# Performance work log

Measured on AMD Instinct MI355X. Metric: run time of the kernel, lower is better.

## Reference

```python
import jax, jax.numpy as jnp
import numpy as np

MASK_FILL = -987654321.0


def rotate_every_two(x):
    # pairs (x0, x1) -> (-x1, x0), interleaved back along last dim
    x1 = x[..., 0::2]
    x2 = x[..., 1::2]
    return jnp.stack((-x2, x1), axis=-1).reshape(x.shape)


def setup_inputs() -> dict:
    key = jax.random.key(0)
    ks = jax.random.split(key, 6)
    b, n, dim = 64, 197, 768
    heads, dim_head = 12, 64
    inner = heads * dim_head
    x = jax.random.normal(ks[0], (b, n, dim), dtype=jnp.float32)
    pos_emb = jax.random.normal(ks[1], (1, n, dim_head), dtype=jnp.float32)
    w_qkv = jax.random.normal(ks[2], (dim, 3 * inner), dtype=jnp.float32) * (dim ** -0.5)
    scale = jnp.full((heads,), dim_head ** -0.5, dtype=jnp.float32)
    w_out = jax.random.normal(ks[3], (inner, dim), dtype=jnp.float32) * (inner ** -0.5)
    b_out = jnp.zeros((dim,), dtype=jnp.float32)
    return {"x": x, "pos_emb": pos_emb, "w_qkv": w_qkv, "scale": scale,
            "w_out": w_out, "b_out": b_out}


def reference(x, pos_emb, w_qkv, scale, w_out, b_out):
    b, n, dim = x.shape
    h = scale.shape[0]
    qkv = x @ w_qkv                         # [b, n, 3*inner]
    q, k, v = jnp.split(qkv, 3, axis=-1)
    dh = q.shape[-1] // h
    to_heads = lambda t: t.reshape(b, n, h, dh).transpose(0, 2, 1, 3)  # bhnd
    q, k, v = to_heads(q), to_heads(k), to_heads(v)

    # RoPE: pos_emb [1, n, (2 * dh/2)] -> sin/cos [n, dh/2] -> interleave to [n, dh]
    sc = pos_emb[0].reshape(n, 2, dh // 2)
    sin = jnp.repeat(sc[:, 0], 2, axis=-1)  # [n, dh]
    cos = jnp.repeat(sc[:, 1], 2, axis=-1)
    q = q * cos + rotate_every_two(q) * sin
    k = k * cos + rotate_every_two(k) * sin

    # per-head learnable scale
    dots = jnp.einsum('bhid,bhjd->bhij', q, k) * scale[None, :, None, None]
    # diagonal (LSA) mask
    eye = jnp.eye(n, dtype=bool)
    dots = jnp.where(eye, MASK_FILL, dots)

    attn = jax.nn.softmax(dots, axis=-1)
    out = jnp.einsum('bhij,bhjd->bhid', attn, v)
    out = out.transpose(0, 2, 1, 3).reshape(b, n, h * dh)
    return out @ w_out + b_out
```

## Files before the change

kernel.cpp:

```cpp
#include <hip/hip_runtime.h>
#include <math.h>

#define MASK_FILL_F (-987654321.0f)

typedef unsigned short u16;
typedef unsigned int   u32;

constexpr int Bb   = 64;
constexpr int Ntok = 197;
constexpr int Dim  = 768;
constexpr int Heads= 12;
constexpr int Dh   = 64;
constexpr int Nq3  = 2304;
constexpr int Rows = 12608;
constexpr int Mpad = 12672;

using f32x4  = __attribute__((ext_vector_type(4))) float;
using bf16x8 = __attribute__((ext_vector_type(8))) short;

__device__ __forceinline__ u16 f2bf(float f) {
  u32 u = __float_as_uint(f);
  u = (u + 0x7fffu + ((u >> 16) & 1u)) >> 16;
  return (u16)u;
}

__device__ __forceinline__ void stage16(const void* gp, void* lp) {
  __builtin_amdgcn_global_load_lds(
      (const __attribute__((address_space(1))) u32*)gp,
      (__attribute__((address_space(3))) u32*)lp, 16, 0, 0);
}

__device__ __forceinline__ int sigma6(int M) {
  return (M & 0x23) | (((M >> 3) & 1) << 4) | (((M >> 2) & 1) << 3) |
         (((M >> 4) & 1) << 2);
}

__global__ __launch_bounds__(256) void cvt_bf16(const float* __restrict__ in,
                                                u16* __restrict__ out, int n4) {
  const int i = blockIdx.x * 256 + threadIdx.x;
  if (i < n4) {
    const float4 v = *(const float4*)&in[(size_t)i * 4];
    ushort4 u;
    u.x = f2bf(v.x); u.y = f2bf(v.y); u.z = f2bf(v.z); u.w = f2bf(v.w);
    *(ushort4*)&out[(size_t)i * 4] = u;
  }
}

__global__ __launch_bounds__(256) void transpose_cvt(const float* __restrict__ in,
                                                     u16* __restrict__ out,
                                                     int R, int C) {
  __shared__ float t[32][33];
  const int c0 = blockIdx.x * 32, r0 = blockIdx.y * 32;
  const int tx = threadIdx.x & 31, ty = threadIdx.x >> 5;
#pragma unroll
  for (int rr = ty; rr < 32; rr += 8)
    t[rr][tx] = in[(size_t)(r0 + rr) * C + c0 + tx];
  __syncthreads();
#pragma unroll
  for (int cc = ty; cc < 32; cc += 8)
    out[(size_t)(c0 + cc) * R + r0 + tx] = f2bf(t[tx][cc]);
}

__global__ __launch_bounds__(256) void vtrans(const u16* __restrict__ qkvB,
                                              u16* __restrict__ vT) {
  __shared__ u16 t[64 * 72];
  const int jt = blockIdx.x, bh = blockIdx.y;
  const int b = bh / Heads, h = bh % Heads;
  const int j0 = jt * 64;
  const int tid = threadIdx.x;

  for (int idx = tid; idx < 512; idx += 256) {
    const int jr = idx >> 3, c8 = (idx & 7) * 8;
    const int j = j0 + jr;
    uint4 u = make_uint4(0u, 0u, 0u, 0u);
    if (j < Ntok)
      u = *(const uint4*)(qkvB + (size_t)(b * Ntok + j) * Nq3 + 2 * Dim + h * Dh + c8);
    *(uint4*)&t[jr * 72 + c8] = u;
  }
  __syncthreads();
  for (int idx = tid; idx < 512; idx += 256) {
    const int d = idx >> 3, j8 = (idx & 7) * 8;
    ushort4 lo, hi;
    lo.x = t[(j8 + 0) * 72 + d]; lo.y = t[(j8 + 1) * 72 + d];
    lo.z = t[(j8 + 2) * 72 + d]; lo.w = t[(j8 + 3) * 72 + d];
    hi.x = t[(j8 + 4) * 72 + d]; hi.y = t[(j8 + 5) * 72 + d];
    hi.z = t[(j8 + 6) * 72 + d]; hi.w = t[(j8 + 7) * 72 + d];
    u16* dst = vT + ((size_t)bh * 64 + d) * 256 + j0 + j8;
    *(ushort4*)dst       = lo;
    *(ushort4*)(dst + 4) = hi;
  }
}

template<int MODE>
__global__ __launch_bounds__(256) void gemm_bt(
    const u16* __restrict__ Ag, const u16* __restrict__ Bg,
    void* __restrict__ Cv, int K, int Nn,
    const float* __restrict__ pe, const float* __restrict__ bias)
{
  __shared__ u16 As[128 * 32];
  __shared__ u16 Bs[128 * 32];
  const int tid = threadIdx.x, lane = tid & 63, w = tid >> 6;
  const int m0 = blockIdx.y * 128, n0 = blockIdx.x * 128;
  const int wm = (w & 1) * 64, wn = (w >> 1) * 64;
  const int tx = lane & 15, qk = lane >> 4;
  const int rs = lane >> 2, cs = (lane & 3) * 8;

  f32x4 acc[4][4] = {};

  for (int k0 = 0; k0 < K; k0 += 32) {
#pragma unroll
    for (int t = 0; t < 2; ++t) {
      const int r0 = w * 16 + t * 64;
      stage16(Ag + (size_t)(m0 + r0 + rs) * K + k0 + cs, &As[r0 * 32]);
      stage16(Bg + (size_t)(n0 + r0 + rs) * K + k0 + cs, &Bs[r0 * 32]);
    }
    __syncthreads();
    bf16x8 af[4], bf[4];
#pragma unroll
    for (int f = 0; f < 4; ++f) {
      af[f] = *(const bf16x8*)&As[(wm + f * 16 + tx) * 32 + qk * 8];
      bf[f] = *(const bf16x8*)&Bs[(wn + f * 16 + tx) * 32 + qk * 8];
    }
#pragma unroll
    for (int fm = 0; fm < 4; ++fm)
#pragma unroll
      for (int fn = 0; fn < 4; ++fn)
        acc[fm][fn] = __builtin_amdgcn_mfma_f32_16x16x32_bf16(
            af[fm], bf[fn], acc[fm][fn], 0, 0, 0);
    __syncthreads();
  }

  if (MODE == 0) {
    u16* C = (u16*)Cv;
    const bool dorot = (n0 < 2 * Dim);
#pragma unroll
    for (int fm = 0; fm < 4; ++fm) {
      const int rbase = m0 + wm + fm * 16 + qk * 4;
      int iq[4];
#pragma unroll
      for (int r = 0; r < 4; ++r) iq[r] = (rbase + r) % Ntok;
#pragma unroll
      for (int fn = 0; fn < 4; ++fn) {
        const int col = n0 + wn + fn * 16 + tx;
        const int mm  = (col & 63) >> 1;
        const int odd = col & 1;
#pragma unroll
        for (int r = 0; r < 4; ++r) {
          float v = acc[fm][fn][r];
          float res = v;
          if (dorot) {
            const float other = __shfl_xor(v, 1, 64);
            const float sn = pe[iq[r] * 64 + mm];
            const float c2 = pe[iq[r] * 64 + 32 + mm];
            res = odd ? (v * c2 + other * sn) : (v * c2 - other * sn);
          }
          C[(size_t)(rbase + r) * Nn + col] = f2bf(res);
        }
      }
    }
  } else {
    float* C = (float*)Cv;
#pragma unroll
    for (int fm = 0; fm < 4; ++fm) {
      const int rbase = m0 + wm + fm * 16 + qk * 4;
#pragma unroll
      for (int fn = 0; fn < 4; ++fn) {
        const int col = n0 + wn + fn * 16 + tx;
        const float bv = bias[col];
#pragma unroll
        for (int r = 0; r < 4; ++r) {
          const int row = rbase + r;
          if (row < Rows) C[(size_t)row * Nn + col] = acc[fm][fn][r] + bv;
        }
      }
    }
  }
}

constexpr int LS = 72;

__global__ __launch_bounds__(256) void attn7(
    const u16* __restrict__ qkvB, const u16* __restrict__ vT,
    const float* __restrict__ scale, u16* __restrict__ outB)
{
  __shared__ u16 ks [64 * LS];
  __shared__ u16 vts[64 * LS];

  const int it = blockIdx.x, bh = blockIdx.y;
  const int b = bh / Heads, h = bh % Heads;
  const int i0 = it * 128;
  const float sc = scale[h];
  const int tid = threadIdx.x, lane = tid & 63, w = tid >> 6;
  const int tx = lane & 15, q = lane >> 4;
  const size_t rowbase = (size_t)b * Ntok;

  bf16x8 bq[2][2];
#pragma unroll
  for (int g = 0; g < 2; ++g)
#pragma unroll
    for (int kk = 0; kk < 2; ++kk)
      bq[g][kk] = *(const bf16x8*)(qkvB +
          (rowbase + i0 + 32 * w + 16 * g + tx) * (size_t)Nq3 + h * Dh + kk * 32 + q * 8);

  float l_part[2] = {0.f, 0.f};
  f32x4 oacc[2][4] = {};

  for (int jt = 0; jt < 4; ++jt) {
    const int j0 = jt * 64;
    __syncthreads();

    for (int idx = tid; idx < 512; idx += 256) {
      const int M = idx >> 3, c8 = (idx & 7) * 8;
      const int js = sigma6(M);
      *(uint4*)&ks[M * LS + c8] =
          *(const uint4*)(qkvB + (rowbase + j0 + js) * (size_t)Nq3 + Dim + h * Dh + c8);
    }
    for (int idx = tid; idx < 512; idx += 256) {
      const int d = idx >> 3, c8 = (idx & 7) * 8;
      *(uint4*)&vts[d * LS + c8] =
          *(const uint4*)(vT + ((size_t)bh * 64 + d) * 256 + j0 + c8);
    }
    __syncthreads();

#pragma unroll
    for (int g = 0; g < 2; ++g) {
      f32x4 sT[4] = {};
#pragma unroll
      for (int kk = 0; kk < 2; ++kk)
#pragma unroll
        for (int jb = 0; jb < 4; ++jb) {
          const bf16x8 ka = *(const bf16x8*)&ks[(jb * 16 + tx) * LS + kk * 32 + q * 8];
          sT[jb] = __builtin_amdgcn_mfma_f32_16x16x32_bf16(ka, bq[g][kk], sT[jb], 0, 0, 0);
        }

      const int ig = i0 + 32 * w + 16 * g + tx;
      union { bf16x8 v; u16 e[8]; } pk[2];
      float lp = 0.f;
#pragma unroll
      for (int jb = 0; jb < 4; ++jb)
#pragma unroll
        for (int r = 0; r < 4; ++r) {
          const int jg = j0 + 32 * (jb >> 1) + 8 * q + 4 * (jb & 1) + r;
          const float s = fminf(sT[jb][r] * sc, 80.f);
          const bool bad = (jg >= Ntok) || (jg == ig);
          const float p = bad ? 0.f : __expf(s);
          lp += p;
          pk[jb >> 1].e[(jb & 1) * 4 + r] = f2bf(p);
        }
      l_part[g] += lp;

#pragma unroll
      for (int kk = 0; kk < 2; ++kk)
#pragma unroll
        for (int nb = 0; nb < 4; ++nb) {
          const bf16x8 vb = *(const bf16x8*)&vts[(nb * 16 + tx) * LS + kk * 32 + q * 8];
          oacc[g][nb] = __builtin_amdgcn_mfma_f32_16x16x32_bf16(pk[kk].v, vb,
                                                               oacc[g][nb], 0, 0, 0);
        }
    }
  }

#pragma unroll
  for (int g = 0; g < 2; ++g) {
    float l = l_part[g];
    l += __shfl_xor(l, 16, 64);
    l += __shfl_xor(l, 32, 64);
    const float linv = 1.0f / l;
#pragma unroll
    for (int r = 0; r < 4; ++r) {
      const float lr = __shfl(linv, 4 * q + r, 64);
      const int igr = i0 + 32 * w + 16 * g + 4 * q + r;
      if (igr < Ntok) {
#pragma unroll
        for (int nb = 0; nb < 4; ++nb)
          outB[(rowbase + igr) * (size_t)Dim + h * Dh + nb * 16 + tx] =
              f2bf(oacc[g][nb][r] * lr);
      }
    }
  }
}

extern "C" void kernel_launch(void* const* d_in, const int* in_sizes, int n_in,
                              void* d_out, int out_size, void* d_ws, size_t ws_size,
                              hipStream_t stream) {
  const float* x     = (const float*)d_in[0];
  const float* pe    = (const float*)d_in[1];
  const float* w_qkv = (const float*)d_in[2];
  const float* scale = (const float*)d_in[3];
  const float* w_out = (const float*)d_in[4];
  const float* b_out = (const float*)d_in[5];
  float* out = (float*)d_out;

  u16* xb    = (u16*)d_ws;
  u16* wqkvT = xb    + (size_t)Mpad * Dim;
  u16* woutT = wqkvT + (size_t)Nq3 * Dim;
  u16* qkvB  = woutT + (size_t)Dim * Dim;
  u16* attnB = qkvB  + (size_t)Mpad * Nq3;
  u16* vT    = attnB + (size_t)Mpad * Dim;

  cvt_bf16<<<(Rows * Dim / 4 + 255) / 256, 256, 0, stream>>>(x, xb, Rows * Dim / 4);
  transpose_cvt<<<dim3(Nq3 / 32, Dim / 32), 256, 0, stream>>>(w_qkv, wqkvT, Dim, Nq3);
  transpose_cvt<<<dim3(Dim / 32, Dim / 32), 256, 0, stream>>>(w_out, woutT, Dim, Dim);

  gemm_bt<0><<<dim3(Nq3 / 128, Mpad / 128), 256, 0, stream>>>(
      xb, wqkvT, qkvB, Dim, Nq3, pe, nullptr);

  vtrans<<<dim3(4, Bb * Heads), 256, 0, stream>>>(qkvB, vT);

  attn7<<<dim3(2, Bb * Heads), 256, 0, stream>>>(qkvB, vT, scale, attnB);

  gemm_bt<1><<<dim3(Dim / 128, Mpad / 128), 256, 0, stream>>>(
      attnB, woutT, out, Dim, Dim, nullptr, b_out);
}
```

Before: 285.4 us.

## Replace bf16 GEMMs with 256x256 double-buffered 8-wave pipelined kernel

```diff
diff --git a/kernel.cpp b/kernel.cpp
--- a/kernel.cpp
+++ b/kernel.cpp
@@ -91,62 +91,140 @@
   }
 }
 
-template<int MODE>
-__global__ __launch_bounds__(256) void gemm_bt(
+constexpr int Kc  = 768;
+constexpr int NKT = Kc / 64;
+
+#define BARM() asm volatile("s_barrier" ::: "memory")
+#define VMW4() asm volatile("s_waitcnt vmcnt(4)" ::: "memory")
+#define VMW2() asm volatile("s_waitcnt vmcnt(2)" ::: "memory")
+#define VMW0() asm volatile("s_waitcnt vmcnt(0)" ::: "memory")
+
+#define PH(MH, NH, RDA, RDB, STG, ...)                                         \
+  do {                                                                         \
+    if (RDA) {                                                                 \
+      _Pragma("unroll") for (int m_ = 0; m_ < 4; ++m_)                         \
+      _Pragma("unroll") for (int k_ = 0; k_ < 2; ++k_)                         \
+        af[m_][k_] = *(const bf16x8*)&Asb[((MH) * 64 + mrow + m_ * 16) * 64    \
+                                          + (((k_ * 4 + qd) ^ sx) * 8)];       \
+    }                                                                          \
+    if (RDB) {                                                                 \
+      _Pragma("unroll") for (int n_ = 0; n_ < 2; ++n_)                         \
+      _Pragma("unroll") for (int k_ = 0; k_ < 2; ++k_)                         \
+        bfr[n_][k_] = *(const bf16x8*)&Bsb[((NH) * 32 + nrow + n_ * 16) * 64   \
+                                           + (((k_ * 4 + qd) ^ sx) * 8)];      \
+    }                                                                          \
+    STG;                                                                       \
+    BARM();                                                                    \
+    __builtin_amdgcn_s_setprio(1);                                             \
+    _Pragma("unroll") for (int m_ = 0; m_ < 4; ++m_)                           \
+    _Pragma("unroll") for (int n_ = 0; n_ < 2; ++n_)                           \
+    _Pragma("unroll") for (int k_ = 0; k_ < 2; ++k_)                           \
+      acc[(MH) * 4 + m_][(NH) * 2 + n_] =                                      \
+          __builtin_amdgcn_mfma_f32_16x16x32_bf16(                             \
+              af[m_][k_], bfr[n_][k_],                                         \
+              acc[(MH) * 4 + m_][(NH) * 2 + n_], 0, 0, 0);                     \
+    __builtin_amdgcn_s_setprio(0);                                             \
+    __VA_ARGS__;                                                               \
+    BARM();                                                                    \
+  } while (0)
+
+template<int MODE, int TN>
+__global__ __launch_bounds__(512, 2) void gemm8p(
     const u16* __restrict__ Ag, const u16* __restrict__ Bg,
-    void* __restrict__ Cv, int K, int Nn,
+    void* __restrict__ Cv, int Nn, int nwg,
     const float* __restrict__ pe, const float* __restrict__ bias)
 {
-  __shared__ u16 As[128 * 32];
-  __shared__ u16 Bs[128 * 32];
+  __shared__ u16 As[2][256 * 64];
+  __shared__ u16 Bs[2][256 * 64];
+
   const int tid = threadIdx.x, lane = tid & 63, w = tid >> 6;
-  const int m0 = blockIdx.y * 128, n0 = blockIdx.x * 128;
-  const int wm = (w & 1) * 64, wn = (w >> 1) * 64;
-  const int tx = lane & 15, qk = lane >> 4;
-  const int rs = lane >> 2, cs = (lane & 3) * 8;
-
-  f32x4 acc[4][4] = {};
-
-  for (int k0 = 0; k0 < K; k0 += 32) {
-#pragma unroll
-    for (int t = 0; t < 2; ++t) {
-      const int r0 = w * 16 + t * 64;
-      stage16(Ag + (size_t)(m0 + r0 + rs) * K + k0 + cs, &As[r0 * 32]);
-      stage16(Bg + (size_t)(n0 + r0 + rs) * K + k0 + cs, &Bs[r0 * 32]);
-    }
-    __syncthreads();
-    bf16x8 af[4], bf[4];
-#pragma unroll
-    for (int f = 0; f < 4; ++f) {
-      af[f] = *(const bf16x8*)&As[(wm + f * 16 + tx) * 32 + qk * 8];
-      bf[f] = *(const bf16x8*)&Bs[(wn + f * 16 + tx) * 32 + qk * 8];
-    }
-#pragma unroll
-    for (int fm = 0; fm < 4; ++fm)
-#pragma unroll
-      for (int fn = 0; fn < 4; ++fn)
-        acc[fm][fn] = __builtin_amdgcn_mfma_f32_16x16x32_bf16(
-            af[fm], bf[fn], acc[fm][fn], 0, 0, 0);
-    __syncthreads();
+
+  const int orig = blockIdx.x;
+  const int q8 = nwg >> 3, r8 = nwg & 7;
+  const int xcd = orig & 7, sub = orig >> 3;
+  const int wgid = (xcd < r8 ? xcd * (q8 + 1) : r8 * (q8 + 1) + (xcd - r8) * q8) + sub;
+  const int tm = wgid / TN, tn = wgid % TN;
+  const int m0 = tm * 256, n0 = tn * 256;
+
+  const int wr = w >> 2, wc = w & 3;
+  const int tx = lane & 15, qd = lane >> 4, sx = tx & 7;
+  const int mrow = wr * 128 + tx, nrow = wc * 64 + tx;
+
+  const int srow = lane >> 3;
+  const int scol = ((lane & 7) ^ srow) * 8;
+  const int a1c = (w & 1) * 16 + (w >> 1) * 2, a2c = a1c + 1;
+  const int a3c = a1c + 8,                     a4c = a2c + 8;
+  const int b1c = (w & 3) * 8 + (w >> 2) * 2,  b2c = b1c + 1;
+  const int b3c = b1c + 4,                     b4c = b2c + 4;
+
+  const u16* sA1 = Ag + (size_t)(m0 + 8 * a1c + srow) * Kc + scol;
+  const u16* sA2 = Ag + (size_t)(m0 + 8 * a2c + srow) * Kc + scol;
+  const u16* sA3 = Ag + (size_t)(m0 + 8 * a3c + srow) * Kc + scol;
+  const u16* sA4 = Ag + (size_t)(m0 + 8 * a4c + srow) * Kc + scol;
+  const u16* sB1 = Bg + (size_t)(n0 + 8 * b1c + srow) * Kc + scol;
+  const u16* sB2 = Bg + (size_t)(n0 + 8 * b2c + srow) * Kc + scol;
+  const u16* sB3 = Bg + (size_t)(n0 + 8 * b3c + srow) * Kc + scol;
+  const u16* sB4 = Bg + (size_t)(n0 + 8 * b4c + srow) * Kc + scol;
+
+  stage16(sA1, &As[0][a1c * 512]); stage16(sB1, &Bs[0][b1c * 512]);
+  stage16(sA2, &As[0][a2c * 512]); stage16(sB2, &Bs[0][b2c * 512]);
+  stage16(sB3, &Bs[0][b3c * 512]); stage16(sB4, &Bs[0][b4c * 512]);
+  stage16(sA3, &As[0][a3c * 512]); stage16(sA4, &As[0][a4c * 512]);
+  sA1 += 64; sA2 += 64; sA3 += 64; sA4 += 64;
+  sB1 += 64; sB2 += 64; sB3 += 64; sB4 += 64;
+  VMW4();
+  BARM();
+
+  f32x4  acc[8][4] = {};
+  bf16x8 af[4][2], bfr[2][2];
+
+  int cur = 0;
+#pragma unroll 1
+  for (int t = 0; t < NKT - 1; ++t) {
+    const u16* Asb = As[cur];
+    const u16* Bsb = Bs[cur];
+    u16* An = As[cur ^ 1];
+    u16* Bn = Bs[cur ^ 1];
+
+    PH(0, 0, 1, 1,
+       { stage16(sA1, &An[a1c * 512]); stage16(sB1, &Bn[b1c * 512]); }, VMW4());
+    PH(0, 1, 0, 1,
+       { stage16(sA2, &An[a2c * 512]); stage16(sB2, &Bn[b2c * 512]); }, VMW4());
+    PH(1, 1, 1, 0,
+       { stage16(sB3, &Bn[b3c * 512]); stage16(sB4, &Bn[b4c * 512]); }, );
+    PH(1, 0, 0, 1,
+       { stage16(sA3, &An[a3c * 512]); stage16(sA4, &An[a4c * 512]); }, VMW4());
+
+    sA1 += 64; sA2 += 64; sA3 += 64; sA4 += 64;
+    sB1 += 64; sB2 += 64; sB3 += 64; sB4 += 64;
+    cur ^= 1;
+  }
+  {
+    const u16* Asb = As[cur];
+    const u16* Bsb = Bs[cur];
+    PH(0, 0, 1, 1, {}, VMW2());
+    PH(0, 1, 0, 1, {}, VMW0());
+    PH(1, 1, 1, 0, {}, );
+    PH(1, 0, 0, 1, {}, );
   }
 
   if (MODE == 0) {
     u16* C = (u16*)Cv;
     const bool dorot = (n0 < 2 * Dim);
 #pragma unroll
-    for (int fm = 0; fm < 4; ++fm) {
-      const int rbase = m0 + wm + fm * 16 + qk * 4;
+    for (int mi = 0; mi < 8; ++mi) {
+      const int rbase = m0 + wr * 128 + mi * 16 + qd * 4;
       int iq[4];
 #pragma unroll
       for (int r = 0; r < 4; ++r) iq[r] = (rbase + r) % Ntok;
 #pragma unroll
-      for (int fn = 0; fn < 4; ++fn) {
-        const int col = n0 + wn + fn * 16 + tx;
+      for (int ni = 0; ni < 4; ++ni) {
+        const int col = n0 + wc * 64 + ni * 16 + tx;
         const int mm  = (col & 63) >> 1;
         const int odd = col & 1;
 #pragma unroll
         for (int r = 0; r < 4; ++r) {
-          float v = acc[fm][fn][r];
+          float v = acc[mi][ni][r];
           float res = v;
           if (dorot) {
             const float other = __shfl_xor(v, 1, 64);
@@ -161,16 +239,16 @@
   } else {
     float* C = (float*)Cv;
 #pragma unroll
-    for (int fm = 0; fm < 4; ++fm) {
-      const int rbase = m0 + wm + fm * 16 + qk * 4;
-#pragma unroll
-      for (int fn = 0; fn < 4; ++fn) {
-        const int col = n0 + wn + fn * 16 + tx;
+    for (int mi = 0; mi < 8; ++mi) {
+      const int rbase = m0 + wr * 128 + mi * 16 + qd * 4;
+#pragma unroll
+      for (int ni = 0; ni < 4; ++ni) {
+        const int col = n0 + wc * 64 + ni * 16 + tx;
         const float bv = bias[col];
 #pragma unroll
         for (int r = 0; r < 4; ++r) {
           const int row = rbase + r;
-          if (row < Rows) C[(size_t)row * Nn + col] = acc[fm][fn][r] + bv;
+          if (row < Rows) C[(size_t)row * Nn + col] = acc[mi][ni][r] + bv;
         }
       }
     }
@@ -302,13 +380,13 @@
   transpose_cvt<<<dim3(Nq3 / 32, Dim / 32), 256, 0, stream>>>(w_qkv, wqkvT, Dim, Nq3);
   transpose_cvt<<<dim3(Dim / 32, Dim / 32), 256, 0, stream>>>(w_out, woutT, Dim, Dim);
 
-  gemm_bt<0><<<dim3(Nq3 / 128, Mpad / 128), 256, 0, stream>>>(
-      xb, wqkvT, qkvB, Dim, Nq3, pe, nullptr);
+  constexpr int NWG0 = 50 * 9;
+  gemm8p<0, 9><<<NWG0, 512, 0, stream>>>(xb, wqkvT, qkvB, Nq3, NWG0, pe, nullptr);
 
   vtrans<<<dim3(4, Bb * Heads), 256, 0, stream>>>(qkvB, vT);
 
   attn7<<<dim3(2, Bb * Heads), 256, 0, stream>>>(qkvB, vT, scale, attnB);
 
-  gemm_bt<1><<<dim3(Dim / 128, Mpad / 128), 256, 0, stream>>>(
-      attnB, woutT, out, Dim, Dim, nullptr, b_out);
-}
+  constexpr int NWG1 = 50 * 3;
+  gemm8p<1, 3><<<NWG1, 512, 0, stream>>>(attnB, woutT, out, Dim, NWG1, nullptr, b_out);
+}
```

New measurement: 284.1 us. Within noise of the previous version (-0.5%).
